# Kernel tuning notes

Hardware: AMD Instinct MI355X
Metric: run time of the kernel (lower is better)

The kernel has to match this reference:

```python
import jax, jax.numpy as jnp
import numpy as np

D_MODEL = 1024
N_HEADS = 16
D_HEAD = D_MODEL // N_HEADS


def setup_inputs() -> dict:
    key = jax.random.key(0)
    k1, k2, k3 = jax.random.split(key, 3)
    B, T = 2, 2048
    x = jax.random.normal(k1, (B, T, D_MODEL), dtype=jnp.float32)
    key_padding_mask = jnp.zeros((B, T), dtype=bool)  # True = padded key
    # nn.Linear weights: [out_features, in_features], bias=False
    W_qkv = jax.random.normal(k2, (3 * D_MODEL, D_MODEL), dtype=jnp.float32) * (D_MODEL ** -0.5)
    W_proj = jax.random.normal(k3, (D_MODEL, D_MODEL), dtype=jnp.float32) * (D_MODEL ** -0.5)
    return {"x": x, "key_padding_mask": key_padding_mask, "W_qkv": W_qkv, "W_proj": W_proj}


def reference(x, key_padding_mask, W_qkv, W_proj):
    B, T, D = x.shape
    H, Dh = N_HEADS, D_HEAD
    scale = Dh ** -0.5
    # qkv: [B,T,3D] -> [3,B,H,T,Dh]
    qkv = (x @ W_qkv.T).reshape(B, T, 3, H, Dh).transpose(2, 0, 3, 1, 4)
    q, k, v = qkv[0], qkv[1], qkv[2]
    # attention scores [B,H,T,T]
    attn = jnp.einsum("bhqd,bhkd->bhqk", q, k) * scale
    attn = jnp.where(key_padding_mask[:, None, None, :], -jnp.inf, attn)
    attn = jax.nn.softmax(attn, axis=-1)  # dropout in eval mode = identity
    out = jnp.einsum("bhqk,bhkd->bhqd", attn, v)
    out = out.transpose(0, 2, 1, 3).reshape(B, T, D)
    return out @ W_proj.T
```

## Files before the change

### kernel.cpp

```cpp
#include <hip/hip_runtime.h>
#include <hip/hip_bf16.h>

typedef unsigned short u16;
typedef unsigned int u32;
typedef __bf16 bf16x8 __attribute__((ext_vector_type(8)));
typedef float f32x4 __attribute__((ext_vector_type(4)));

#define DMODEL 1024
#define NH 16
#define DH 64
#define BB 2
#define TT 2048
#define MM 4096
#define NQKV 3072
#define KVB 64

#define QSCALE 0.18033688011112042f

static __device__ __forceinline__ u16 f2bf(float f) {
  u32 u = __float_as_uint(f);
  u = (u + 0x7FFFu + ((u >> 16) & 1u)) >> 16;
  return (u16)u;
}

static __device__ __forceinline__ u32 pk2bf(float a, float b) {
  u16 ua = __builtin_bit_cast(u16, (__bf16)a);
  u16 ub = __builtin_bit_cast(u16, (__bf16)b);
  return (u32)ua | ((u32)ub << 16);
}

static __device__ __forceinline__ float fexp2(float x) {
#if __has_builtin(__builtin_amdgcn_exp2f)
  return __builtin_amdgcn_exp2f(x);
#else
  float r; asm("v_exp_f32 %0, %1" : "=v"(r) : "v"(x)); return r;
#endif
}

static __device__ __forceinline__ float max3f(float a, float b, float c) {
  return fmaxf(fmaxf(a, b), c);
}

static __device__ __forceinline__ void gload16(const u16* g, u16* l) {
  __builtin_amdgcn_global_load_lds(
      (const __attribute__((address_space(1))) void*)g,
      (__attribute__((address_space(3))) void*)l, 16, 0, 0);
}

__global__ __launch_bounds__(256) void cvt_bf16_4(const float* __restrict__ src,
                                                  u16* __restrict__ dst, int n4) {
  int i = blockIdx.x * 256 + threadIdx.x;
  if (i >= n4) return;
  float4 v = reinterpret_cast<const float4*>(src)[i];
  ushort4 o;
  o.x = f2bf(v.x); o.y = f2bf(v.y); o.z = f2bf(v.z); o.w = f2bf(v.w);
  reinterpret_cast<ushort4*>(dst)[i] = o;
}

static __device__ __forceinline__ void gemm_stage(
    const u16* __restrict__ A, const u16* __restrict__ B, u16* As, u16* Bs,
    int r0, int o0, int r1, int o1, int c0, int c1, int kcol) {
  gload16(A + (size_t)r0 * DMODEL + kcol + o0, As + c0 * 8);
  gload16(A + (size_t)r1 * DMODEL + kcol + o1, As + c1 * 8);
  gload16(B + (size_t)r0 * DMODEL + kcol + o0, Bs + c0 * 8);
  gload16(B + (size_t)r1 * DMODEL + kcol + o1, Bs + c1 * 8);
}

static __device__ __forceinline__ void gemm128_mainloop(
    const u16* __restrict__ Abase, const u16* __restrict__ Bbase,
    u16* As, u16* Bs, f32x4 (&acc)[4][4]) {
  const int tid = threadIdx.x;
  const int lane = tid & 63;
  const int w = tid >> 6;
  const int rowg = lane >> 4, col = lane & 15;
  const int wm = w >> 1, wn = w & 1;
  const int c0 = tid, c1 = tid + 256;
  const int r0 = c0 >> 2, o0 = (c0 & 3) * 8;
  const int r1 = c1 >> 2, o1 = (c1 & 3) * 8;

  gemm_stage(Abase, Bbase, As, Bs, r0, o0, r1, o1, c0, c1, 0);
  asm volatile("s_waitcnt vmcnt(0)" ::: "memory");
  __builtin_amdgcn_s_barrier();

  int sel = 0;
  for (int kt = 0; kt < DMODEL / 32; ++kt) {
    const int kn = ((kt + 1) & (DMODEL / 32 - 1)) * 32;
    const int ns = sel ^ 1;
    gemm_stage(Abase, Bbase, As + ns * 4096, Bs + ns * 4096, r0, o0, r1, o1, c0, c1, kn);
    const u16* as = As + sel * 4096;
    const u16* bs = Bs + sel * 4096;
    bf16x8 af[4], bfr[4];
#pragma unroll
    for (int i = 0; i < 4; ++i)
      af[i] = *reinterpret_cast<const bf16x8*>(as + (wm * 64 + i * 16 + col) * 32 + rowg * 8);
#pragma unroll
    for (int j = 0; j < 4; ++j)
      bfr[j] = *reinterpret_cast<const bf16x8*>(bs + (wn * 64 + j * 16 + col) * 32 + rowg * 8);
#pragma unroll
    for (int i = 0; i < 4; ++i)
#pragma unroll
      for (int j = 0; j < 4; ++j)
        acc[i][j] = __builtin_amdgcn_mfma_f32_16x16x32_bf16(af[i], bfr[j], acc[i][j], 0, 0, 0);
    asm volatile("s_waitcnt vmcnt(0)" ::: "memory");
    __builtin_amdgcn_s_barrier();
    sel = ns;
  }
}

__global__ __launch_bounds__(256, 3) void qkv_gemm(
    const u16* __restrict__ xb, const u16* __restrict__ wb,
    u16* __restrict__ qb, u16* __restrict__ kb, u16* __restrict__ vtb) {
  __shared__ u16 As[2 * 128 * 32];
  __shared__ u16 Bs[2 * 128 * 32];
  f32x4 acc[4][4];
#pragma unroll
  for (int i = 0; i < 4; ++i)
#pragma unroll
    for (int j = 0; j < 4; ++j) acc[i][j] = (f32x4){0.f, 0.f, 0.f, 0.f};
  gemm128_mainloop(xb + (size_t)blockIdx.y * 128 * DMODEL,
                   wb + (size_t)blockIdx.x * 128 * DMODEL, As, Bs, acc);
  const int lane = threadIdx.x & 63, w = threadIdx.x >> 6;
  const int rowg = lane >> 4, col = lane & 15, wm = w >> 1, wn = w & 1;
#pragma unroll
  for (int i = 0; i < 4; ++i) {
#pragma unroll
    for (int j = 0; j < 4; ++j) {
#pragma unroll
      for (int r = 0; r < 4; ++r) {
        int m = blockIdx.y * 128 + wm * 64 + i * 16 + rowg * 4 + r;
        int n = blockIdx.x * 128 + wn * 64 + j * 16 + col;
        int b = m >> 11, t = m & (TT - 1);
        int s = n >> 10, h = (n >> 6) & 15, d = n & 63;
        int bh = b * NH + h;
        float v = acc[i][j][r];
        if (s == 0)      qb[((size_t)bh * TT + t) * DH + d] = f2bf(v * QSCALE);
        else if (s == 1) kb[((size_t)bh * TT + t) * DH + d] = f2bf(v);
        else             vtb[((size_t)bh * DH + d) * TT + t] = f2bf(v);
      }
    }
  }
}

__global__ __launch_bounds__(256, 3) void proj_gemm(
    const u16* __restrict__ ab, const u16* __restrict__ wb, float* __restrict__ out) {
  __shared__ u16 As[2 * 128 * 32];
  __shared__ u16 Bs[2 * 128 * 32];
  f32x4 acc[4][4];
#pragma unroll
  for (int i = 0; i < 4; ++i)
#pragma unroll
    for (int j = 0; j < 4; ++j) acc[i][j] = (f32x4){0.f, 0.f, 0.f, 0.f};
  gemm128_mainloop(ab + (size_t)blockIdx.y * 128 * DMODEL,
                   wb + (size_t)blockIdx.x * 128 * DMODEL, As, Bs, acc);
  const int lane = threadIdx.x & 63, w = threadIdx.x >> 6;
  const int rowg = lane >> 4, col = lane & 15, wm = w >> 1, wn = w & 1;
#pragma unroll
  for (int i = 0; i < 4; ++i) {
#pragma unroll
    for (int j = 0; j < 4; ++j) {
#pragma unroll
      for (int r = 0; r < 4; ++r) {
        int m = blockIdx.y * 128 + wm * 64 + i * 16 + rowg * 4 + r;
        int n = blockIdx.x * 128 + wn * 64 + j * 16 + col;
        out[(size_t)m * DMODEL + n] = acc[i][j][r];
      }
    }
  }
}

static __device__ __forceinline__ void attn_stage(
    const u16* __restrict__ kbase, const u16* __restrict__ vbase,
    int kt, u16* KsSel, u16* VsSel, int tid) {
#pragma unroll
  for (int p = 0; p < 2; ++p) {
    int c = p * 256 + tid;
    int row = c >> 3;
    int bI = (c & 7) * 16;
    gload16(kbase + kt * (KVB * DH) + row * DH + ((bI ^ ((row & 7) << 4)) >> 1), KsSel + c * 8);
  }
#pragma unroll
  for (int p = 0; p < 2; ++p) {
    int c = p * 256 + tid;
    int d = c >> 3;
    int bI = (c & 7) * 16;
    gload16(vbase + (size_t)d * TT + kt * KVB + ((bI ^ ((d & 7) << 4)) >> 1), VsSel + c * 8);
  }
}

__global__ __launch_bounds__(256, 2) void attn_kernel(
    const u16* __restrict__ qb, const u16* __restrict__ kb,
    const u16* __restrict__ vtb, const unsigned char* __restrict__ mask,
    u16* __restrict__ ob) {
  __shared__ u16 Ks[2][KVB * DH];
  __shared__ u16 Vs[2][DH * KVB];
  __shared__ u16 Pl[4][32 * KVB];
  __shared__ unsigned char maskb[TT];
  __shared__ u32 mflag;

  const int tid = threadIdx.x;
  const int lane = tid & 63, w = tid >> 6;
  const int rowg = lane >> 4, col = lane & 15;
  const int qt = blockIdx.x, bh = blockIdx.y;
  const int b = bh >> 4;

  if (tid == 0) mflag = 0;
  __syncthreads();

  {
    const u32* mg = reinterpret_cast<const u32*>(mask + (size_t)b * TT);
    u32 m0 = mg[tid * 2], m1 = mg[tid * 2 + 1];
    *reinterpret_cast<u32*>(maskb + tid * 8) = m0;
    *reinterpret_cast<u32*>(maskb + tid * 8 + 4) = m1;
    if (m0 | m1) atomicOr(&mflag, 1u << (tid >> 3));
  }

  const int qrow0 = qt * 128 + w * 32;
  const u16* qptr = qb + ((size_t)bh * TT + qrow0) * DH;
  bf16x8 a_q[2][2];
#pragma unroll
  for (int qg = 0; qg < 2; ++qg)
#pragma unroll
    for (int ds = 0; ds < 2; ++ds)
      a_q[qg][ds] = *reinterpret_cast<const bf16x8*>(qptr + (qg * 16 + col) * DH + ds * 32 + rowg * 8);

  f32x4 acc_o[2][4];
  float m_run[2], l_run[2];
#pragma unroll
  for (int qg = 0; qg < 2; ++qg) {
#pragma unroll
    for (int df = 0; df < 4; ++df) acc_o[qg][df] = (f32x4){0.f, 0.f, 0.f, 0.f};
    m_run[qg] = -1e30f; l_run[qg] = 0.f;
  }

  const u16* kbase = kb + (size_t)bh * TT * DH;
  const u16* vbase = vtb + (size_t)bh * DH * TT;
  u16* pw = Pl[w];

  attn_stage(kbase, vbase, 0, Ks[0], Vs[0], tid);
  __syncthreads();
  const u32 fm = mflag;

  int cur = 0;
  for (int t = 0; t < TT / KVB; ++t) {
    const int tn = (t + 1) & (TT / KVB - 1);
    attn_stage(kbase, vbase, tn, Ks[cur ^ 1], Vs[cur ^ 1], tid);

    f32x4 sc[2][4];
#pragma unroll
    for (int qg = 0; qg < 2; ++qg)
#pragma unroll
      for (int kf = 0; kf < 4; ++kf) sc[qg][kf] = (f32x4){0.f, 0.f, 0.f, 0.f};
    const u16* ks = Ks[cur];
#pragma unroll
    for (int ds = 0; ds < 2; ++ds) {
      bf16x8 ak[4];
#pragma unroll
      for (int kf = 0; kf < 4; ++kf) {
        int krow = kf * 16 + col;
        ak[kf] = *reinterpret_cast<const bf16x8*>(
            ks + krow * DH + (((ds * 64 + rowg * 16) ^ ((krow & 7) << 4)) >> 1));
      }
#pragma unroll
      for (int qg = 0; qg < 2; ++qg)
#pragma unroll
        for (int kf = 0; kf < 4; ++kf)
          sc[qg][kf] = __builtin_amdgcn_mfma_f32_16x16x32_bf16(ak[kf], a_q[qg][ds], sc[qg][kf], 0, 0, 0);
    }

    if (fm & (1u << t)) {
#pragma unroll
      for (int kf = 0; kf < 4; ++kf)
#pragma unroll
        for (int r = 0; r < 4; ++r) {
          float ma = maskb[t * KVB + kf * 16 + rowg * 4 + r] ? -1e30f : 0.f;
          sc[0][kf][r] += ma;
          sc[1][kf][r] += ma;
        }
    }

#pragma unroll
    for (int qg = 0; qg < 2; ++qg) {
      float t0 = max3f(sc[qg][0][0], sc[qg][0][1], sc[qg][0][2]);
      float t1 = max3f(sc[qg][0][3], sc[qg][1][0], sc[qg][1][1]);
      float t2 = max3f(sc[qg][1][2], sc[qg][1][3], sc[qg][2][0]);
      float t3 = max3f(sc[qg][2][1], sc[qg][2][2], sc[qg][2][3]);
      float t4 = max3f(sc[qg][3][0], sc[qg][3][1], sc[qg][3][2]);
      float mx = fmaxf(max3f(t0, t1, t2), max3f(t3, t4, sc[qg][3][3]));
      mx = fmaxf(mx, __shfl_xor(mx, 16, 64));
      mx = fmaxf(mx, __shfl_xor(mx, 32, 64));
      if (__any(mx > m_run[qg] + 8.0f)) {
        float mn = fmaxf(m_run[qg], mx);
        float corr = fexp2(m_run[qg] - mn);
        m_run[qg] = mn;
        l_run[qg] *= corr;
#pragma unroll
        for (int df = 0; df < 4; ++df) acc_o[qg][df] *= corr;
      }
      const float mc = m_run[qg];

      const int q = qg * 16 + col;
      const int sw = (q & 7) << 4;
      u16* prow = pw + q * KVB;
      float rs = 0.f;
#pragma unroll
      for (int kf = 0; kf < 4; ++kf) {
        float p0 = fexp2(sc[qg][kf][0] - mc);
        float p1 = fexp2(sc[qg][kf][1] - mc);
        float p2 = fexp2(sc[qg][kf][2] - mc);
        float p3 = fexp2(sc[qg][kf][3] - mc);
        rs += (p0 + p1) + (p2 + p3);
        uint2 pk;
        pk.x = pk2bf(p0, p1);
        pk.y = pk2bf(p2, p3);
        int bI = kf * 32 + rowg * 8;
        *reinterpret_cast<uint2*>(prow + ((bI ^ sw) >> 1)) = pk;
      }
      rs += __shfl_xor(rs, 16, 64);
      rs += __shfl_xor(rs, 32, 64);
      l_run[qg] += rs;
    }
    asm volatile("s_waitcnt lgkmcnt(0)" ::: "memory");
    __builtin_amdgcn_sched_barrier(0);

    const u16* vs = Vs[cur];
    __builtin_amdgcn_s_setprio(1);
#pragma unroll
    for (int ksI = 0; ksI < 2; ++ksI) {
      bf16x8 bp[2];
#pragma unroll
      for (int qg = 0; qg < 2; ++qg) {
        int q = qg * 16 + col;
        bp[qg] = *reinterpret_cast<const bf16x8*>(
            pw + q * KVB + (((ksI * 64 + rowg * 16) ^ ((q & 7) << 4)) >> 1));
      }
#pragma unroll
      for (int df = 0; df < 4; ++df) {
        int vrow = df * 16 + col;
        bf16x8 bv = *reinterpret_cast<const bf16x8*>(
            vs + vrow * KVB + (((ksI * 64 + rowg * 16) ^ ((vrow & 7) << 4)) >> 1));
#pragma unroll
        for (int qg = 0; qg < 2; ++qg)
          acc_o[qg][df] = __builtin_amdgcn_mfma_f32_16x16x32_bf16(bv, bp[qg], acc_o[qg][df], 0, 0, 0);
      }
    }
    __builtin_amdgcn_s_setprio(0);

    asm volatile("s_waitcnt vmcnt(0)" ::: "memory");
    __builtin_amdgcn_s_barrier();
    cur ^= 1;
  }

  const int h = bh & 15;
#pragma unroll
  for (int qg = 0; qg < 2; ++qg) {
    float inv = 1.f / l_run[qg];
    int tq = qrow0 + qg * 16 + col;
    size_t rowoff = ((size_t)(b * TT + tq)) * DMODEL + h * DH + rowg * 4;
#pragma unroll
    for (int df = 0; df < 4; ++df) {
      ushort4 o4;
      o4.x = f2bf(acc_o[qg][df][0] * inv);
      o4.y = f2bf(acc_o[qg][df][1] * inv);
      o4.z = f2bf(acc_o[qg][df][2] * inv);
      o4.w = f2bf(acc_o[qg][df][3] * inv);
      *reinterpret_cast<ushort4*>(ob + rowoff + df * 16) = o4;
    }
  }
}

extern "C" void kernel_launch(void* const* d_in, const int* in_sizes, int n_in,
                              void* d_out, int out_size, void* d_ws, size_t ws_size,
                              hipStream_t stream) {
  const float* x = (const float*)d_in[0];
  const unsigned char* mask = (const unsigned char*)d_in[1];
  const float* wqkv = (const float*)d_in[2];
  const float* wproj = (const float*)d_in[3];
  float* out = (float*)d_out;

  u16* xb     = (u16*)d_ws;
  u16* wqkvb  = xb    + (size_t)MM * DMODEL;
  u16* wprojb = wqkvb + (size_t)NQKV * DMODEL;
  u16* qb     = wprojb + (size_t)DMODEL * DMODEL;
  u16* kb     = qb + (size_t)MM * DMODEL;
  u16* vtb    = kb + (size_t)MM * DMODEL;
  u16* ob     = vtb + (size_t)MM * DMODEL;

  cvt_bf16_4<<<MM * DMODEL / 4 / 256, 256, 0, stream>>>(x, xb, MM * DMODEL / 4);
  cvt_bf16_4<<<NQKV * DMODEL / 4 / 256, 256, 0, stream>>>(wqkv, wqkvb, NQKV * DMODEL / 4);
  cvt_bf16_4<<<DMODEL * DMODEL / 4 / 256, 256, 0, stream>>>(wproj, wprojb, DMODEL * DMODEL / 4);

  qkv_gemm<<<dim3(NQKV / 128, MM / 128), 256, 0, stream>>>(xb, wqkvb, qb, kb, vtb);
  attn_kernel<<<dim3(TT / 128, BB * NH), 256, 0, stream>>>(qb, kb, vtb, mask, ob);
  proj_gemm<<<dim3(DMODEL / 128, MM / 128), 256, 0, stream>>>(ob, wprojb, out);
}
```

Baseline: 143.0 us.

## Triple-buffer GEMM and attention loads, fuse the three bf16 convert kernels

```diff
diff --git a/kernel.cpp b/kernel.cpp
--- a/kernel.cpp
+++ b/kernel.cpp
@@ -47,11 +47,24 @@
       (__attribute__((address_space(3))) void*)l, 16, 0, 0);
 }
 
-__global__ __launch_bounds__(256) void cvt_bf16_4(const float* __restrict__ src,
-                                                  u16* __restrict__ dst, int n4) {
+#define N4X  (MM * DMODEL / 4)
+#define N4W  (NQKV * DMODEL / 4)
+#define N4P  (DMODEL * DMODEL / 4)
+__global__ __launch_bounds__(256) void cvt_all(const float* __restrict__ x,
+                                               const float* __restrict__ wqkv,
+                                               const float* __restrict__ wproj,
+                                               u16* __restrict__ dst) {
   int i = blockIdx.x * 256 + threadIdx.x;
-  if (i >= n4) return;
-  float4 v = reinterpret_cast<const float4*>(src)[i];
+  const float* src;
+  int j = i;
+  if (i < N4X) {
+    src = x;
+  } else if (i < N4X + N4W) {
+    src = wqkv; j = i - N4X;
+  } else {
+    src = wproj; j = i - (N4X + N4W);
+  }
+  float4 v = reinterpret_cast<const float4*>(src)[j];
   ushort4 o;
   o.x = f2bf(v.x); o.y = f2bf(v.y); o.z = f2bf(v.z); o.w = f2bf(v.w);
   reinterpret_cast<ushort4*>(dst)[i] = o;
@@ -79,16 +92,16 @@
   const int r1 = c1 >> 2, o1 = (c1 & 3) * 8;
 
   gemm_stage(Abase, Bbase, As, Bs, r0, o0, r1, o1, c0, c1, 0);
-  asm volatile("s_waitcnt vmcnt(0)" ::: "memory");
+  gemm_stage(Abase, Bbase, As + 4096, Bs + 4096, r0, o0, r1, o1, c0, c1, 32);
+  asm volatile("s_waitcnt vmcnt(4)" ::: "memory");
   __builtin_amdgcn_s_barrier();
 
-  int sel = 0;
   for (int kt = 0; kt < DMODEL / 32; ++kt) {
-    const int kn = ((kt + 1) & (DMODEL / 32 - 1)) * 32;
-    const int ns = sel ^ 1;
-    gemm_stage(Abase, Bbase, As + ns * 4096, Bs + ns * 4096, r0, o0, r1, o1, c0, c1, kn);
-    const u16* as = As + sel * 4096;
-    const u16* bs = Bs + sel * 4096;
+    const int kn = ((kt + 2) & (DMODEL / 32 - 1)) * 32;
+    const int sp = ((kt + 2) % 3) * 4096;
+    gemm_stage(Abase, Bbase, As + sp, Bs + sp, r0, o0, r1, o1, c0, c1, kn);
+    const u16* as = As + (kt % 3) * 4096;
+    const u16* bs = Bs + (kt % 3) * 4096;
     bf16x8 af[4], bfr[4];
 #pragma unroll
     for (int i = 0; i < 4; ++i)
@@ -101,17 +114,16 @@
 #pragma unroll
       for (int j = 0; j < 4; ++j)
         acc[i][j] = __builtin_amdgcn_mfma_f32_16x16x32_bf16(af[i], bfr[j], acc[i][j], 0, 0, 0);
-    asm volatile("s_waitcnt vmcnt(0)" ::: "memory");
+    asm volatile("s_waitcnt vmcnt(4)" ::: "memory");
     __builtin_amdgcn_s_barrier();
-    sel = ns;
   }
 }
 
 __global__ __launch_bounds__(256, 3) void qkv_gemm(
     const u16* __restrict__ xb, const u16* __restrict__ wb,
     u16* __restrict__ qb, u16* __restrict__ kb, u16* __restrict__ vtb) {
-  __shared__ u16 As[2 * 128 * 32];
-  __shared__ u16 Bs[2 * 128 * 32];
+  __shared__ u16 As[3 * 128 * 32];
+  __shared__ u16 Bs[3 * 128 * 32];
   f32x4 acc[4][4];
 #pragma unroll
   for (int i = 0; i < 4; ++i)
@@ -143,8 +155,8 @@
 
 __global__ __launch_bounds__(256, 3) void proj_gemm(
     const u16* __restrict__ ab, const u16* __restrict__ wb, float* __restrict__ out) {
-  __shared__ u16 As[2 * 128 * 32];
-  __shared__ u16 Bs[2 * 128 * 32];
+  __shared__ u16 As[3 * 128 * 32];
+  __shared__ u16 Bs[3 * 128 * 32];
   f32x4 acc[4][4];
 #pragma unroll
   for (int i = 0; i < 4; ++i)
@@ -191,8 +203,8 @@
     const u16* __restrict__ qb, const u16* __restrict__ kb,
     const u16* __restrict__ vtb, const unsigned char* __restrict__ mask,
     u16* __restrict__ ob) {
-  __shared__ u16 Ks[2][KVB * DH];
-  __shared__ u16 Vs[2][DH * KVB];
+  __shared__ u16 Ks[3][KVB * DH];
+  __shared__ u16 Vs[3][DH * KVB];
   __shared__ u16 Pl[4][32 * KVB];
   __shared__ unsigned char maskb[TT];
   __shared__ u32 mflag;
@@ -237,20 +249,22 @@
   u16* pw = Pl[w];
 
   attn_stage(kbase, vbase, 0, Ks[0], Vs[0], tid);
+  attn_stage(kbase, vbase, 1, Ks[1], Vs[1], tid);
+  asm volatile("s_waitcnt vmcnt(4)" ::: "memory");
   __syncthreads();
   const u32 fm = mflag;
 
-  int cur = 0;
   for (int t = 0; t < TT / KVB; ++t) {
-    const int tn = (t + 1) & (TT / KVB - 1);
-    attn_stage(kbase, vbase, tn, Ks[cur ^ 1], Vs[cur ^ 1], tid);
+    const int tn2 = (t + 2) & (TT / KVB - 1);
+    const int sp = (t + 2) % 3;
+    attn_stage(kbase, vbase, tn2, Ks[sp], Vs[sp], tid);
 
     f32x4 sc[2][4];
 #pragma unroll
     for (int qg = 0; qg < 2; ++qg)
 #pragma unroll
       for (int kf = 0; kf < 4; ++kf) sc[qg][kf] = (f32x4){0.f, 0.f, 0.f, 0.f};
-    const u16* ks = Ks[cur];
+    const u16* ks = Ks[t % 3];
 #pragma unroll
     for (int ds = 0; ds < 2; ++ds) {
       bf16x8 ak[4];
@@ -322,7 +336,7 @@
     asm volatile("s_waitcnt lgkmcnt(0)" ::: "memory");
     __builtin_amdgcn_sched_barrier(0);
 
-    const u16* vs = Vs[cur];
+    const u16* vs = Vs[t % 3];
     __builtin_amdgcn_s_setprio(1);
 #pragma unroll
     for (int ksI = 0; ksI < 2; ++ksI) {
@@ -345,9 +359,8 @@
     }
     __builtin_amdgcn_s_setprio(0);
 
-    asm volatile("s_waitcnt vmcnt(0)" ::: "memory");
+    asm volatile("s_waitcnt vmcnt(4)" ::: "memory");
     __builtin_amdgcn_s_barrier();
-    cur ^= 1;
   }
 
   const int h = bh & 15;
@@ -385,10 +398,7 @@
   u16* vtb    = kb + (size_t)MM * DMODEL;
   u16* ob     = vtb + (size_t)MM * DMODEL;
 
-  cvt_bf16_4<<<MM * DMODEL / 4 / 256, 256, 0, stream>>>(x, xb, MM * DMODEL / 4);
-  cvt_bf16_4<<<NQKV * DMODEL / 4 / 256, 256, 0, stream>>>(wqkv, wqkvb, NQKV * DMODEL / 4);
-  cvt_bf16_4<<<DMODEL * DMODEL / 4 / 256, 256, 0, stream>>>(wproj, wprojb, DMODEL * DMODEL / 4);
-
+  cvt_all<<<(N4X + N4W + N4P) / 256, 256, 0, stream>>>(x, wqkv, wproj, xb);
   qkv_gemm<<<dim3(NQKV / 128, MM / 128), 256, 0, stream>>>(xb, wqkvb, qb, kb, vtb);
   attn_kernel<<<dim3(TT / 128, BB * NH), 256, 0, stream>>>(qb, kb, vtb, mask, ob);
   proj_gemm<<<dim3(DMODEL / 128, MM / 128), 256, 0, stream>>>(ob, wprojb, out);
```

Result: slower. 147.4 us (+3.0%).

## Use 8 waves of 16 query rows in attention and fuse bf16 conversions

Applied to the files above, without the earlier changes.

```diff
diff --git a/kernel.cpp b/kernel.cpp
--- a/kernel.cpp
+++ b/kernel.cpp
@@ -47,11 +47,24 @@
       (__attribute__((address_space(3))) void*)l, 16, 0, 0);
 }
 
-__global__ __launch_bounds__(256) void cvt_bf16_4(const float* __restrict__ src,
-                                                  u16* __restrict__ dst, int n4) {
+#define N4X  (MM * DMODEL / 4)
+#define N4W  (NQKV * DMODEL / 4)
+#define N4P  (DMODEL * DMODEL / 4)
+__global__ __launch_bounds__(256) void cvt_all(const float* __restrict__ x,
+                                               const float* __restrict__ wqkv,
+                                               const float* __restrict__ wproj,
+                                               u16* __restrict__ dst) {
   int i = blockIdx.x * 256 + threadIdx.x;
-  if (i >= n4) return;
-  float4 v = reinterpret_cast<const float4*>(src)[i];
+  const float* src;
+  int j = i;
+  if (i < N4X) {
+    src = x;
+  } else if (i < N4X + N4W) {
+    src = wqkv; j = i - N4X;
+  } else {
+    src = wproj; j = i - (N4X + N4W);
+  }
+  float4 v = reinterpret_cast<const float4*>(src)[j];
   ushort4 o;
   o.x = f2bf(v.x); o.y = f2bf(v.y); o.z = f2bf(v.z); o.w = f2bf(v.w);
   reinterpret_cast<ushort4*>(dst)[i] = o;
@@ -171,29 +184,19 @@
 static __device__ __forceinline__ void attn_stage(
     const u16* __restrict__ kbase, const u16* __restrict__ vbase,
     int kt, u16* KsSel, u16* VsSel, int tid) {
-#pragma unroll
-  for (int p = 0; p < 2; ++p) {
-    int c = p * 256 + tid;
-    int row = c >> 3;
-    int bI = (c & 7) * 16;
-    gload16(kbase + kt * (KVB * DH) + row * DH + ((bI ^ ((row & 7) << 4)) >> 1), KsSel + c * 8);
-  }
-#pragma unroll
-  for (int p = 0; p < 2; ++p) {
-    int c = p * 256 + tid;
-    int d = c >> 3;
-    int bI = (c & 7) * 16;
-    gload16(vbase + (size_t)d * TT + kt * KVB + ((bI ^ ((d & 7) << 4)) >> 1), VsSel + c * 8);
-  }
-}
-
-__global__ __launch_bounds__(256, 2) void attn_kernel(
+  int row = tid >> 3;
+  int bI = (tid & 7) * 16;
+  gload16(kbase + kt * (KVB * DH) + row * DH + ((bI ^ ((row & 7) << 4)) >> 1), KsSel + tid * 8);
+  gload16(vbase + (size_t)row * TT + kt * KVB + ((bI ^ ((row & 7) << 4)) >> 1), VsSel + tid * 8);
+}
+
+__global__ __launch_bounds__(512, 2) void attn_kernel(
     const u16* __restrict__ qb, const u16* __restrict__ kb,
     const u16* __restrict__ vtb, const unsigned char* __restrict__ mask,
     u16* __restrict__ ob) {
   __shared__ u16 Ks[2][KVB * DH];
   __shared__ u16 Vs[2][DH * KVB];
-  __shared__ u16 Pl[4][32 * KVB];
+  __shared__ u16 Pl[8][16 * KVB];
   __shared__ unsigned char maskb[TT];
   __shared__ u32 mflag;
 
@@ -207,30 +210,22 @@
   __syncthreads();
 
   {
-    const u32* mg = reinterpret_cast<const u32*>(mask + (size_t)b * TT);
-    u32 m0 = mg[tid * 2], m1 = mg[tid * 2 + 1];
-    *reinterpret_cast<u32*>(maskb + tid * 8) = m0;
-    *reinterpret_cast<u32*>(maskb + tid * 8 + 4) = m1;
-    if (m0 | m1) atomicOr(&mflag, 1u << (tid >> 3));
-  }
-
-  const int qrow0 = qt * 128 + w * 32;
+    u32 m0 = reinterpret_cast<const u32*>(mask + (size_t)b * TT)[tid];
+    *reinterpret_cast<u32*>(maskb + tid * 4) = m0;
+    if (m0) atomicOr(&mflag, 1u << (tid >> 4));
+  }
+
+  const int qrow0 = qt * 128 + w * 16;
   const u16* qptr = qb + ((size_t)bh * TT + qrow0) * DH;
-  bf16x8 a_q[2][2];
-#pragma unroll
-  for (int qg = 0; qg < 2; ++qg)
-#pragma unroll
-    for (int ds = 0; ds < 2; ++ds)
-      a_q[qg][ds] = *reinterpret_cast<const bf16x8*>(qptr + (qg * 16 + col) * DH + ds * 32 + rowg * 8);
-
-  f32x4 acc_o[2][4];
-  float m_run[2], l_run[2];
-#pragma unroll
-  for (int qg = 0; qg < 2; ++qg) {
-#pragma unroll
-    for (int df = 0; df < 4; ++df) acc_o[qg][df] = (f32x4){0.f, 0.f, 0.f, 0.f};
-    m_run[qg] = -1e30f; l_run[qg] = 0.f;
-  }
+  bf16x8 a_q[2];
+#pragma unroll
+  for (int ds = 0; ds < 2; ++ds)
+    a_q[ds] = *reinterpret_cast<const bf16x8*>(qptr + col * DH + ds * 32 + rowg * 8);
+
+  f32x4 acc_o[4];
+  float m_run = -1e30f, l_run = 0.f;
+#pragma unroll
+  for (int df = 0; df < 4; ++df) acc_o[df] = (f32x4){0.f, 0.f, 0.f, 0.f};
 
   const u16* kbase = kb + (size_t)bh * TT * DH;
   const u16* vbase = vtb + (size_t)bh * DH * TT;
@@ -245,11 +240,9 @@
     const int tn = (t + 1) & (TT / KVB - 1);
     attn_stage(kbase, vbase, tn, Ks[cur ^ 1], Vs[cur ^ 1], tid);
 
-    f32x4 sc[2][4];
-#pragma unroll
-    for (int qg = 0; qg < 2; ++qg)
-#pragma unroll
-      for (int kf = 0; kf < 4; ++kf) sc[qg][kf] = (f32x4){0.f, 0.f, 0.f, 0.f};
+    f32x4 sc[4];
+#pragma unroll
+    for (int kf = 0; kf < 4; ++kf) sc[kf] = (f32x4){0.f, 0.f, 0.f, 0.f};
     const u16* ks = Ks[cur];
 #pragma unroll
     for (int ds = 0; ds < 2; ++ds) {
@@ -261,53 +254,46 @@
             ks + krow * DH + (((ds * 64 + rowg * 16) ^ ((krow & 7) << 4)) >> 1));
       }
 #pragma unroll
-      for (int qg = 0; qg < 2; ++qg)
-#pragma unroll
-        for (int kf = 0; kf < 4; ++kf)
-          sc[qg][kf] = __builtin_amdgcn_mfma_f32_16x16x32_bf16(ak[kf], a_q[qg][ds], sc[qg][kf], 0, 0, 0);
+      for (int kf = 0; kf < 4; ++kf)
+        sc[kf] = __builtin_amdgcn_mfma_f32_16x16x32_bf16(ak[kf], a_q[ds], sc[kf], 0, 0, 0);
     }
 
     if (fm & (1u << t)) {
 #pragma unroll
       for (int kf = 0; kf < 4; ++kf)
 #pragma unroll
-        for (int r = 0; r < 4; ++r) {
-          float ma = maskb[t * KVB + kf * 16 + rowg * 4 + r] ? -1e30f : 0.f;
-          sc[0][kf][r] += ma;
-          sc[1][kf][r] += ma;
-        }
-    }
-
-#pragma unroll
-    for (int qg = 0; qg < 2; ++qg) {
-      float t0 = max3f(sc[qg][0][0], sc[qg][0][1], sc[qg][0][2]);
-      float t1 = max3f(sc[qg][0][3], sc[qg][1][0], sc[qg][1][1]);
-      float t2 = max3f(sc[qg][1][2], sc[qg][1][3], sc[qg][2][0]);
-      float t3 = max3f(sc[qg][2][1], sc[qg][2][2], sc[qg][2][3]);
-      float t4 = max3f(sc[qg][3][0], sc[qg][3][1], sc[qg][3][2]);
-      float mx = fmaxf(max3f(t0, t1, t2), max3f(t3, t4, sc[qg][3][3]));
+        for (int r = 0; r < 4; ++r)
+          sc[kf][r] += maskb[t * KVB + kf * 16 + rowg * 4 + r] ? -1e30f : 0.f;
+    }
+
+    {
+      float t0 = max3f(sc[0][0], sc[0][1], sc[0][2]);
+      float t1 = max3f(sc[0][3], sc[1][0], sc[1][1]);
+      float t2 = max3f(sc[1][2], sc[1][3], sc[2][0]);
+      float t3 = max3f(sc[2][1], sc[2][2], sc[2][3]);
+      float t4 = max3f(sc[3][0], sc[3][1], sc[3][2]);
+      float mx = fmaxf(max3f(t0, t1, t2), max3f(t3, t4, sc[3][3]));
       mx = fmaxf(mx, __shfl_xor(mx, 16, 64));
       mx = fmaxf(mx, __shfl_xor(mx, 32, 64));
-      if (__any(mx > m_run[qg] + 8.0f)) {
-        float mn = fmaxf(m_run[qg], mx);
-        float corr = fexp2(m_run[qg] - mn);
-        m_run[qg] = mn;
-        l_run[qg] *= corr;
-#pragma unroll
-        for (int df = 0; df < 4; ++df) acc_o[qg][df] *= corr;
-      }
-      const float mc = m_run[qg];
-
-      const int q = qg * 16 + col;
-      const int sw = (q & 7) << 4;
-      u16* prow = pw + q * KVB;
+      if (__any(mx > m_run + 8.0f)) {
+        float mn = fmaxf(m_run, mx);
+        float corr = fexp2(m_run - mn);
+        m_run = mn;
+        l_run *= corr;
+#pragma unroll
+        for (int df = 0; df < 4; ++df) acc_o[df] *= corr;
+      }
+      const float mc = m_run;
+
+      const int sw = (col & 7) << 4;
+      u16* prow = pw + col * KVB;
       float rs = 0.f;
 #pragma unroll
       for (int kf = 0; kf < 4; ++kf) {
-        float p0 = fexp2(sc[qg][kf][0] - mc);
-        float p1 = fexp2(sc[qg][kf][1] - mc);
-        float p2 = fexp2(sc[qg][kf][2] - mc);
-        float p3 = fexp2(sc[qg][kf][3] - mc);
+        float p0 = fexp2(sc[kf][0] - mc);
+        float p1 = fexp2(sc[kf][1] - mc);
+        float p2 = fexp2(sc[kf][2] - mc);
+        float p3 = fexp2(sc[kf][3] - mc);
         rs += (p0 + p1) + (p2 + p3);
         uint2 pk;
         pk.x = pk2bf(p0, p1);
@@ -317,7 +303,7 @@
       }
       rs += __shfl_xor(rs, 16, 64);
       rs += __shfl_xor(rs, 32, 64);
-      l_run[qg] += rs;
+      l_run += rs;
     }
     asm volatile("s_waitcnt lgkmcnt(0)" ::: "memory");
     __builtin_amdgcn_sched_barrier(0);
@@ -326,21 +312,14 @@
     __builtin_amdgcn_s_setprio(1);
 #pragma unroll
     for (int ksI = 0; ksI < 2; ++ksI) {
-      bf16x8 bp[2];
-#pragma unroll
-      for (int qg = 0; qg < 2; ++qg) {
-        int q = qg * 16 + col;
-        bp[qg] = *reinterpret_cast<const bf16x8*>(
-            pw + q * KVB + (((ksI * 64 + rowg * 16) ^ ((q & 7) << 4)) >> 1));
-      }
+      bf16x8 bp = *reinterpret_cast<const bf16x8*>(
+          pw + col * KVB + (((ksI * 64 + rowg * 16) ^ ((col & 7) << 4)) >> 1));
 #pragma unroll
       for (int df = 0; df < 4; ++df) {
         int vrow = df * 16 + col;
         bf16x8 bv = *reinterpret_cast<const bf16x8*>(
             vs + vrow * KVB + (((ksI * 64 + rowg * 16) ^ ((vrow & 7) << 4)) >> 1));
-#pragma unroll
-        for (int qg = 0; qg < 2; ++qg)
-          acc_o[qg][df] = __builtin_amdgcn_mfma_f32_16x16x32_bf16(bv, bp[qg], acc_o[qg][df], 0, 0, 0);
+        acc_o[df] = __builtin_amdgcn_mfma_f32_16x16x32_bf16(bv, bp, acc_o[df], 0, 0, 0);
       }
     }
     __builtin_amdgcn_s_setprio(0);
@@ -351,18 +330,17 @@
   }
 
   const int h = bh & 15;
-#pragma unroll
-  for (int qg = 0; qg < 2; ++qg) {
-    float inv = 1.f / l_run[qg];
-    int tq = qrow0 + qg * 16 + col;
+  {
+    float inv = 1.f / l_run;
+    int tq = qrow0 + col;
     size_t rowoff = ((size_t)(b * TT + tq)) * DMODEL + h * DH + rowg * 4;
 #pragma unroll
     for (int df = 0; df < 4; ++df) {
       ushort4 o4;
-      o4.x = f2bf(acc_o[qg][df][0] * inv);
-      o4.y = f2bf(acc_o[qg][df][1] * inv);
-      o4.z = f2bf(acc_o[qg][df][2] * inv);
-      o4.w = f2bf(acc_o[qg][df][3] * inv);
+      o4.x = f2bf(acc_o[df][0] * inv);
+      o4.y = f2bf(acc_o[df][1] * inv);
+      o4.z = f2bf(acc_o[df][2] * inv);
+      o4.w = f2bf(acc_o[df][3] * inv);
       *reinterpret_cast<ushort4*>(ob + rowoff + df * 16) = o4;
     }
   }
@@ -385,11 +363,8 @@
   u16* vtb    = kb + (size_t)MM * DMODEL;
   u16* ob     = vtb + (size_t)MM * DMODEL;
 
-  cvt_bf16_4<<<MM * DMODEL / 4 / 256, 256, 0, stream>>>(x, xb, MM * DMODEL / 4);
-  cvt_bf16_4<<<NQKV * DMODEL / 4 / 256, 256, 0, stream>>>(wqkv, wqkvb, NQKV * DMODEL / 4);
-  cvt_bf16_4<<<DMODEL * DMODEL / 4 / 256, 256, 0, stream>>>(wproj, wprojb, DMODEL * DMODEL / 4);
-
+  cvt_all<<<(N4X + N4W + N4P) / 256, 256, 0, stream>>>(x, wqkv, wproj, xb);
   qkv_gemm<<<dim3(NQKV / 128, MM / 128), 256, 0, stream>>>(xb, wqkvb, qb, kb, vtb);
-  attn_kernel<<<dim3(TT / 128, BB * NH), 256, 0, stream>>>(qb, kb, vtb, mask, ob);
+  attn_kernel<<<dim3(TT / 128, BB * NH), 512, 0, stream>>>(qb, kb, vtb, mask, ob);
   proj_gemm<<<dim3(DMODEL / 128, MM / 128), 256, 0, stream>>>(ob, wprojb, out);
 }
```

New measurement: 135.1 us. -5.5%, faster.
